# Performance work log

Measured on AMD Instinct MI355X. Metric: run time of the kernel, lower is better.

## Reference

```python
import jax, jax.numpy as jnp
import numpy as np

NU = 50000   # num user nodes
NI = 50000   # num item nodes
E = 1600000  # edges per relation
DIN = 256    # in_features
H = 8        # n_heads
F = 64       # out_features per head (hidden = H*F = 512)
NEG_SLOPE = 0.2


def setup_inputs() -> dict:
    key = jax.random.key(0)
    ks = jax.random.split(key, 14)
    wscale = 0.05
    return {
        "x_user": jax.random.normal(ks[0], (NU, DIN), jnp.float32),
        "x_item": jax.random.normal(ks[1], (NI, DIN), jnp.float32),
        "Wv": jax.random.normal(ks[2], (3, DIN, H * F), jnp.float32) * wscale,
        "bv": jax.random.normal(ks[3], (3, H * F), jnp.float32) * wscale,
        "Wq": jax.random.normal(ks[4], (3, H * F, H), jnp.float32) * wscale,
        "bq": jax.random.normal(ks[5], (3, H), jnp.float32) * wscale,
        "Wk": jax.random.normal(ks[6], (3, H * F, H), jnp.float32) * wscale,
        "bk": jax.random.normal(ks[7], (3, H), jnp.float32) * wscale,
        "src1": jax.random.randint(ks[8], (E,), 0, NU, jnp.int32),   # user -> item
        "dst1": jax.random.randint(ks[9], (E,), 0, NI, jnp.int32),
        "src2": jax.random.randint(ks[10], (E,), 0, NI, jnp.int32),  # item -> user
        "dst2": jax.random.randint(ks[11], (E,), 0, NU, jnp.int32),
        "src3": jax.random.randint(ks[12], (E,), 0, NU, jnp.int32),  # user -> user
        "dst3": jax.random.randint(ks[13], (E,), 0, NU, jnp.int32),
    }


def _gat_relation(x_src, x_dst, Wv, bv, Wq, bq, Wk, bk, src, dst, n_dst):
    # linear_v on src and dst node features: [N, H*F]
    h_src = x_src @ Wv + bv
    h_dst = x_dst @ Wv + bv
    q = h_dst @ Wq + bq  # [Nd, H] per-head query logit
    k = h_src @ Wk + bk  # [Ns, H] per-head key logit
    # fused_gsddmm: gather to edges, leaky_relu, segment softmax over dst
    e = jax.nn.leaky_relu(q[dst] + k[src], NEG_SLOPE)  # [E, H]
    m = jax.ops.segment_max(e, dst, num_segments=n_dst)  # [Nd, H]
    m = jnp.where(jnp.isfinite(m), m, jnp.zeros_like(m))
    ex = jnp.exp(e - m[dst])
    denom = jax.ops.segment_sum(ex, dst, num_segments=n_dst)  # [Nd, H]
    attn = ex / jnp.maximum(denom[dst], 1e-9)  # [E, H]
    # gspmm: attention-weighted scatter-sum of src features into dst
    hs = h_src.reshape(-1, H, F)  # [Ns, H, F]
    agg = jax.ops.segment_sum(attn[:, :, None] * hs[src], dst, num_segments=n_dst)  # [Nd, H, F]
    return agg.mean(axis=1)  # torch.mean(h, dim=1) -> [Nd, F]


def reference(x_user, x_item, Wv, bv, Wq, bq, Wk, bk, src1, dst1, src2, dst2, src3, dst3):
    # relation 0: user -> item
    out_item = _gat_relation(x_user, x_item, Wv[0], bv[0], Wq[0], bq[0], Wk[0], bk[0], src1, dst1, NI)
    # relations 1 (item -> user) and 2 (user -> user) both target user: mean over relations
    r1 = _gat_relation(x_item, x_user, Wv[1], bv[1], Wq[1], bq[1], Wk[1], bk[1], src2, dst2, NU)
    r2 = _gat_relation(x_user, x_user, Wv[2], bv[2], Wq[2], bq[2], Wk[2], bk[2], src3, dst3, NU)
    out_user = (r1 + r2) / 2.0
    return out_user, out_item
```

## Files before the change

### kernel.cpp

```cpp
#include <hip/hip_runtime.h>

typedef unsigned short u16;
typedef __attribute__((ext_vector_type(4))) float f32x4;
typedef __attribute__((ext_vector_type(8))) short s16x8;

#define NND 50000
#define EDG 1600000
#define NBK 391
#define TOTB (3 * NBK)
#define TS 4096

__device__ __forceinline__ u16 f2b(float f) {
  union { float f; unsigned u; } c; c.f = f;
  unsigned r = c.u + 0x7fff + ((c.u >> 16) & 1);
  return (u16)(r >> 16);
}
__device__ __forceinline__ float b2f(u16 b) {
  union { float f; unsigned u; } c; c.u = ((unsigned)b) << 16; return c.f;
}

__global__ void k_zero(int* p, int n) {
  int i = blockIdx.x * 256 + threadIdx.x;
  if (i < n) p[i] = 0;
}

__global__ void k_prepw(const float* __restrict__ Wv, u16* __restrict__ Wt) {
  int tid = blockIdx.x * 256 + threadIdx.x;
  if (tid < 3 * 512 * 256) {
    int r = tid / (512 * 256); int rem = tid - r * 512 * 256;
    int n = rem >> 8; int kk = rem & 255;
    Wt[tid] = f2b(Wv[((size_t)r * 256 + kk) * 512 + n]);
  }
}

__global__ void k_fusew(const float* __restrict__ Wv, const float* __restrict__ bv,
                        const float* __restrict__ Wq, const float* __restrict__ bq,
                        const float* __restrict__ Wk, const float* __restrict__ bk,
                        float* __restrict__ FW, float* __restrict__ FB) {
  int tid = blockIdx.x * 256 + threadIdx.x;
  if (tid < 3 * 16 * 256) {
    int r = tid >> 12, o = (tid >> 8) & 15, kk = tid & 255;
    const float* wv = Wv + ((size_t)r * 256 + kk) * 512;
    const float* wqk = (o < 8) ? (Wq + r * 512 * 8 + o) : (Wk + r * 512 * 8 + (o - 8));
    float s = 0.f;
    for (int j = 0; j < 512; j++) s += wv[j] * wqk[j * 8];
    FW[tid] = s;
  }
  if (tid < 48) {
    int r = tid / 16, o = tid % 16;
    const float* wqk = (o < 8) ? (Wq + r * 512 * 8 + o) : (Wk + r * 512 * 8 + (o - 8));
    const float* bvp = bv + r * 512;
    float s = (o < 8) ? bq[r * 8 + o] : bk[r * 8 + (o - 8)];
    for (int j = 0; j < 512; j++) s += bvp[j] * wqk[j * 8];
    FB[tid] = s;
  }
}


__global__ void kb_count(const int* __restrict__ d1, const int* __restrict__ d2,
                         const int* __restrict__ d3, int* __restrict__ BC) {
  __shared__ int h[NBK];
  int tid = threadIdx.x;
  int r = blockIdx.y;
  const int* d = (r == 0) ? d1 : (r == 1) ? d2 : d3;
  for (int b = tid; b < NBK; b += 256) h[b] = 0;
  __syncthreads();
  for (int e = blockIdx.x * 256 + tid; e < EDG; e += 256 * gridDim.x)
    atomicAdd(&h[d[e] >> 7], 1);
  __syncthreads();
  for (int b = tid; b < NBK; b += 256)
    if (h[b]) atomicAdd(&BC[r * NBK + b], h[b]);
}

__global__ void kb_scan(const int* __restrict__ BC, int* __restrict__ BB,
                        int* __restrict__ BCUR, int* __restrict__ rp) {
  __shared__ int a[2][2048];
  int t = threadIdx.x;
  a[0][t]        = (t < TOTB) ? BC[t] : 0;
  a[0][t + 1024] = (t + 1024 < TOTB) ? BC[t + 1024] : 0;
  __syncthreads();
  int s = 0;
  for (int off = 1; off < 2048; off <<= 1) {
    int v0 = a[s][t];        if (t >= off) v0 += a[s][t - off];
    int v1 = a[s][t + 1024]; if (t + 1024 >= off) v1 += a[s][t + 1024 - off];
    __syncthreads();
    a[s ^ 1][t] = v0; a[s ^ 1][t + 1024] = v1;
    __syncthreads();
    s ^= 1;
  }
  if (t < TOTB)        { int e = a[s][t] - BC[t];               BB[t] = e;        BCUR[t] = e; }
  if (t + 1024 < TOTB) { int e = a[s][t + 1024] - BC[t + 1024]; BB[t + 1024] = e; BCUR[t + 1024] = e; }
  if (t == 0) rp[3 * NND] = 3 * EDG;
}

__global__ void __launch_bounds__(256) kb_scatter(
    const int* __restrict__ s1, const int* __restrict__ d1,
    const int* __restrict__ s2, const int* __restrict__ d2,
    const int* __restrict__ s3, const int* __restrict__ d3,
    int* __restrict__ BCUR, unsigned* __restrict__ pairs) {
  __shared__ int h[NBK];
  __shared__ int bbase[NBK];
  int tid = threadIdx.x;
  int r = blockIdx.y;
  const int* dp = (r == 0) ? d1 : (r == 1) ? d2 : d3;
  const int* sp = (r == 0) ? s1 : (r == 1) ? s2 : s3;
  int e0 = blockIdx.x * TS;
  int n = EDG - e0; if (n > TS) n = TS;
  for (int b = tid; b < NBK; b += 256) h[b] = 0;
  __syncthreads();
  int eb[16]; unsigned ev[16];
#pragma unroll
  for (int k = 0; k < 16; k++) {
    int i = k * 256 + tid;
    if (i < n) {
      int d = dp[e0 + i], ss = sp[e0 + i];
      eb[k] = d >> 7;
      ev[k] = ((unsigned)(d & 127) << 16) | (unsigned)ss;
      atomicAdd(&h[eb[k]], 1);
    } else eb[k] = -1;
  }
  __syncthreads();
  for (int b = tid; b < NBK; b += 256) {
    int c = h[b];
    bbase[b] = c ? atomicAdd(&BCUR[r * NBK + b], c) : 0;
  }
  __syncthreads();
  for (int b = tid; b < NBK; b += 256) h[b] = 0;
  __syncthreads();
#pragma unroll
  for (int k = 0; k < 16; k++) {
    if (eb[k] >= 0) {
      int off = atomicAdd(&h[eb[k]], 1);
      pairs[bbase[eb[k]] + off] = ev[k];
    }
  }
}

__global__ void __launch_bounds__(256) kb_build(
    const unsigned* __restrict__ pairs, const int* __restrict__ BB,
    const int* __restrict__ BC, int* __restrict__ rp, int* __restrict__ csrc) {
  __shared__ int cntl[128];
  __shared__ int sc[128];
  __shared__ int curl[128];
  int t = threadIdx.x;
  int r = blockIdx.y, bx = blockIdx.x;
  int bin = r * NBK + bx;
  int base = BB[bin], cnt = BC[bin];
  int node0 = bx << 7;
  int nloc = NND - node0; if (nloc > 128) nloc = 128;
  if (t < 128) cntl[t] = 0;
  __syncthreads();
  for (int i = t; i < cnt; i += 256)
    atomicAdd(&cntl[pairs[base + i] >> 16], 1);
  __syncthreads();
  if (t < 128) sc[t] = cntl[t];
  __syncthreads();
  for (int off = 1; off < 128; off <<= 1) {
    int v = 0;
    if (t < 128) { v = sc[t]; if (t >= off) v += sc[t - off]; }
    __syncthreads();
    if (t < 128) sc[t] = v;
    __syncthreads();
  }
  if (t < 128) {
    int excl = sc[t] - cntl[t];
    if (t < nloc) rp[r * NND + node0 + t] = base + excl;
    curl[t] = base + excl;
  }
  __syncthreads();
  for (int i = t; i < cnt; i += 256) {
    unsigned v = pairs[base + i];
    int p = atomicAdd(&curl[v >> 16], 1);
    csrc[p] = (int)(v & 0xFFFFu);
  }
}

__global__ void __launch_bounds__(256) k_gemm(const float* __restrict__ A, const u16* __restrict__ Bt,
                                              const float* __restrict__ bias, u16* __restrict__ C, int M) {
  __shared__ u16 sA[128 * 40];
  __shared__ u16 sB[128 * 40];
  int tid = threadIdx.x;
  int lane = tid & 63, wid = tid >> 6;
  int wm = wid >> 1, wn = wid & 1;
  int l15 = lane & 15, l4 = lane >> 4;
  int m0 = blockIdx.x * 128, n0 = blockIdx.y * 128;
  f32x4 acc[4][4] = {};
  for (int ko = 0; ko < 256; ko += 32) {
#pragma unroll
    for (int p = 0; p < 2; p++) {
      int idx = p * 256 + tid;
      int row = idx >> 2, seg = idx & 3;
      int gm = m0 + row; if (gm >= M) gm = M - 1;
      float4 a0 = *(const float4*)(A + (size_t)gm * 256 + ko + seg * 8);
      float4 a1 = *(const float4*)(A + (size_t)gm * 256 + ko + seg * 8 + 4);
      s16x8 av;
      av[0] = (short)f2b(a0.x); av[1] = (short)f2b(a0.y);
      av[2] = (short)f2b(a0.z); av[3] = (short)f2b(a0.w);
      av[4] = (short)f2b(a1.x); av[5] = (short)f2b(a1.y);
      av[6] = (short)f2b(a1.z); av[7] = (short)f2b(a1.w);
      *(s16x8*)&sA[row * 40 + seg * 8] = av;
      *(s16x8*)&sB[row * 40 + seg * 8] = *(const s16x8*)(Bt + (n0 + row) * 256 + ko + seg * 8);
    }
    __syncthreads();
    s16x8 af[4], bf[4];
#pragma unroll
    for (int i = 0; i < 4; i++) af[i] = *(const s16x8*)&sA[(wm * 64 + i * 16 + l15) * 40 + l4 * 8];
#pragma unroll
    for (int j = 0; j < 4; j++) bf[j] = *(const s16x8*)&sB[(wn * 64 + j * 16 + l15) * 40 + l4 * 8];
#pragma unroll
    for (int i = 0; i < 4; i++)
#pragma unroll
      for (int j = 0; j < 4; j++)
        acc[i][j] = __builtin_amdgcn_mfma_f32_16x16x32_bf16(af[i], bf[j], acc[i][j], 0, 0, 0);
    __syncthreads();
  }
#pragma unroll
  for (int j = 0; j < 4; j++) {
    int n = n0 + wn * 64 + j * 16 + l15;
    float bb = bias[n];
#pragma unroll
    for (int i = 0; i < 4; i++) {
      int mb = m0 + wm * 64 + i * 16 + l4 * 4;
#pragma unroll
      for (int r = 0; r < 4; r++) {
        int m = mb + r;
        if (m < M) C[(size_t)m * 512 + n] = f2b(acc[i][j][r] + bb);
      }
    }
  }
}

__global__ void k_qk(const float* __restrict__ x, const float* __restrict__ FW,
                     const float* __restrict__ FB, float* __restrict__ qout,
                     float* __restrict__ kout, int N) {
  int lane = threadIdx.x & 63, wid = threadIdx.x >> 6;
  int stride = gridDim.x * 4;
  for (int row = blockIdx.x * 4 + wid; row < N; row += stride) {
    float4 xv = *(const float4*)(x + (size_t)row * 256 + lane * 4);
    float p[16];
#pragma unroll
    for (int o = 0; o < 16; o++) {
      float4 wv = *(const float4*)(FW + o * 256 + lane * 4);
      p[o] = xv.x * wv.x + xv.y * wv.y + xv.z * wv.z + xv.w * wv.w;
    }
#pragma unroll
    for (int off = 1; off < 64; off <<= 1)
#pragma unroll
      for (int o = 0; o < 16; o++) p[o] += __shfl_xor(p[o], off, 64);
    if (lane == 0) {
      if (qout) {
#pragma unroll
        for (int o = 0; o < 8; o++) qout[row * 8 + o] = p[o] + FB[o];
      }
      if (kout) {
#pragma unroll
        for (int o = 0; o < 8; o++) kout[row * 8 + o] = p[o + 8] + FB[o + 8];
      }
    }
  }
}

__global__ void __launch_bounds__(256) k_edge(const int* __restrict__ rp, const int* __restrict__ csrc,
                       const float* __restrict__ q, const float* __restrict__ k,
                       const u16* __restrict__ hs, float* __restrict__ out,
                       float scale, int accum) {
  __shared__ float exw[4][64 * 8];
  __shared__ int sarr[4][64];
  int lane = threadIdx.x & 63, w = threadIdx.x >> 6;
  int dst = blockIdx.x * 4 + w;
  if (dst >= NND) return;
  int beg = rp[dst];
  int deg = rp[dst + 1] - beg;
  float qv[8];
  {
    float4 q0 = *(const float4*)(q + dst * 8);
    float4 q1 = *(const float4*)(q + dst * 8 + 4);
    qv[0] = q0.x; qv[1] = q0.y; qv[2] = q0.z; qv[3] = q0.w;
    qv[4] = q1.x; qv[5] = q1.y; qv[6] = q1.z; qv[7] = q1.w;
  }
  float dsum[8] = {0, 0, 0, 0, 0, 0, 0, 0};
  for (int base = 0; base < deg; base += 64) {
    int i = base + lane;
    if (i < deg) {
      int s = csrc[beg + i];
      float4 k0 = *(const float4*)(k + s * 8);
      float4 k1 = *(const float4*)(k + s * 8 + 4);
      float kv[8] = {k0.x, k0.y, k0.z, k0.w, k1.x, k1.y, k1.z, k1.w};
#pragma unroll
      for (int h = 0; h < 8; h++) {
        float e = qv[h] + kv[h];
        e = e > 0.f ? e : 0.2f * e;
        dsum[h] += exp2f(e * 1.44269504f);
      }
    }
  }
#pragma unroll
  for (int off = 1; off < 64; off <<= 1)
#pragma unroll
    for (int h = 0; h < 8; h++) dsum[h] += __shfl_xor(dsum[h], off, 64);
  float rden[8];
#pragma unroll
  for (int h = 0; h < 8; h++) rden[h] = dsum[h] > 0.f ? 1.f / dsum[h] : 0.f;

  float acc8[8] = {0, 0, 0, 0, 0, 0, 0, 0};
  for (int base = 0; base < deg; base += 64) {
    int i = base + lane;
    int nn = min(64, deg - base);
    if (i < deg) {
      int s = csrc[beg + i];
      sarr[w][lane] = s;
      float4 k0 = *(const float4*)(k + s * 8);
      float4 k1 = *(const float4*)(k + s * 8 + 4);
      float kv[8] = {k0.x, k0.y, k0.z, k0.w, k1.x, k1.y, k1.z, k1.w};
#pragma unroll
      for (int h = 0; h < 8; h++) {
        float e = qv[h] + kv[h];
        e = e > 0.f ? e : 0.2f * e;
        exw[w][lane * 8 + h] = exp2f(e * 1.44269504f) * rden[h];
      }
    }
    __asm__ __volatile__("s_waitcnt lgkmcnt(0)" ::: "memory");
    for (int j = 0; j < nn; j++) {
      int s = sarr[w][j];
      const u16* hp = hs + (size_t)s * 512 + lane;
      float4 e0 = *(const float4*)&exw[w][j * 8];
      float4 e1 = *(const float4*)&exw[w][j * 8 + 4];
      acc8[0] += e0.x * b2f(hp[0 * 64]);
      acc8[1] += e0.y * b2f(hp[1 * 64]);
      acc8[2] += e0.z * b2f(hp[2 * 64]);
      acc8[3] += e0.w * b2f(hp[3 * 64]);
      acc8[4] += e1.x * b2f(hp[4 * 64]);
      acc8[5] += e1.y * b2f(hp[5 * 64]);
      acc8[6] += e1.z * b2f(hp[6 * 64]);
      acc8[7] += e1.w * b2f(hp[7 * 64]);
    }
  }
  float acc = ((acc8[0] + acc8[1]) + (acc8[2] + acc8[3])) + ((acc8[4] + acc8[5]) + (acc8[6] + acc8[7]));
  acc *= scale;
  if (accum) out[dst * 64 + lane] += acc;
  else out[dst * 64 + lane] = acc;
}

extern "C" void kernel_launch(void* const* d_in, const int* in_sizes, int n_in,
                              void* d_out, int out_size, void* d_ws, size_t ws_size,
                              hipStream_t stream) {
  const float* xu = (const float*)d_in[0];
  const float* xi = (const float*)d_in[1];
  const float* Wv = (const float*)d_in[2];
  const float* bv = (const float*)d_in[3];
  const float* Wq = (const float*)d_in[4];
  const float* bq = (const float*)d_in[5];
  const float* Wk = (const float*)d_in[6];
  const float* bk = (const float*)d_in[7];
  const int* src1 = (const int*)d_in[8];
  const int* dst1 = (const int*)d_in[9];
  const int* src2 = (const int*)d_in[10];
  const int* dst2 = (const int*)d_in[11];
  const int* src3 = (const int*)d_in[12];
  const int* dst3 = (const int*)d_in[13];
  float* out_user = (float*)d_out;
  float* out_item = out_user + (size_t)NND * 64;

  char* w = (char*)d_ws;
  auto alloc = [&](size_t sz) -> char* {
    char* p = w; w += (sz + 255) & ~(size_t)255; return p;
  };
  u16* H    = (u16*)alloc((size_t)NND * 512 * 2);
  u16* WT   = (u16*)alloc((size_t)3 * 512 * 256 * 2);
  float* FW = (float*)alloc((size_t)3 * 16 * 256 * 4);
  float* FB = (float*)alloc((size_t)3 * 16 * 4);
  float* Q0 = (float*)alloc((size_t)NND * 8 * 4);
  float* K0 = (float*)alloc((size_t)NND * 8 * 4);
  float* Q1 = (float*)alloc((size_t)NND * 8 * 4);
  float* K1 = (float*)alloc((size_t)NND * 8 * 4);
  float* Q2 = (float*)alloc((size_t)NND * 8 * 4);
  float* K2 = (float*)alloc((size_t)NND * 8 * 4);
  int* ROWPTR = (int*)alloc(((size_t)3 * NND + 1) * 4);
  int* BC   = (int*)alloc(TOTB * 4);
  int* BB   = (int*)alloc(TOTB * 4);
  int* BCUR = (int*)alloc(TOTB * 4);
  int* CSRC = (int*)alloc((size_t)3 * EDG * 4);
  unsigned* PAIRS = (unsigned*)H;
  (void)ws_size; (void)n_in; (void)in_sizes; (void)out_size;

  k_zero<<<(TOTB + 255) / 256, 256, 0, stream>>>(BC, TOTB);
  kb_count<<<dim3(256, 3), 256, 0, stream>>>(dst1, dst2, dst3, BC);
  kb_scan<<<1, 1024, 0, stream>>>(BC, BB, BCUR, ROWPTR);
  kb_scatter<<<dim3((EDG + TS - 1) / TS, 3), 256, 0, stream>>>(src1, dst1, src2, dst2, src3, dst3, BCUR, PAIRS);
  kb_build<<<dim3(NBK, 3), 256, 0, stream>>>(PAIRS, BB, BC, ROWPTR, CSRC);

  k_prepw<<<(3 * 512 * 256 + 255) / 256, 256, 0, stream>>>(Wv, WT);
  k_fusew<<<48, 256, 0, stream>>>(Wv, bv, Wq, bq, Wk, bk, FW, FB);

  k_qk<<<1024, 256, 0, stream>>>(xi, FW,        FB,      Q0, nullptr, NND);
  k_qk<<<1024, 256, 0, stream>>>(xu, FW,        FB,      nullptr, K0, NND);
  k_qk<<<1024, 256, 0, stream>>>(xu, FW + 4096, FB + 16, Q1, nullptr, NND);
  k_qk<<<1024, 256, 0, stream>>>(xi, FW + 4096, FB + 16, nullptr, K1, NND);
  k_qk<<<1024, 256, 0, stream>>>(xu, FW + 8192, FB + 32, Q2, K2, NND);

  dim3 gg((NND + 127) / 128, 4);
  k_gemm<<<gg, 256, 0, stream>>>(xu, WT,                 bv,        H, NND);
  k_edge<<<NND / 4, 256, 0, stream>>>(ROWPTR,           CSRC, Q0, K0, H, out_item, 0.125f,  0);
  k_gemm<<<gg, 256, 0, stream>>>(xi, WT + 512 * 256,     bv + 512,  H, NND);
  k_edge<<<NND / 4, 256, 0, stream>>>(ROWPTR + NND,     CSRC, Q1, K1, H, out_user, 0.0625f, 0);
  k_gemm<<<gg, 256, 0, stream>>>(xu, WT + 2 * 512 * 256, bv + 1024, H, NND);
  k_edge<<<NND / 4, 256, 0, stream>>>(ROWPTR + 2 * NND, CSRC, Q2, K2, H, out_user, 0.0625f, 1);
}
```

Measured before the change: 1.279 ms.

## Sort CSR bins in LDS, interleave GEMM output heads, fuse q/k projections

kb_build now loads each destination bin into shared memory and bitonic-sorts it, so CSR sources come out in deterministic sorted order; the old atomic path is kept as a fallback for oversized bins. The GEMM writes its output with head and feature interleaved, so each lane in k_edge can fetch its 8 per-head bf16 values with one 16-byte load instead of eight strided 2-byte loads. The five q/k projection launches are merged into two kernels, one per input matrix, so x_user and x_item are each read once. The bitonic sort adds many barrier-separated passes in kb_build, and the 32-output k_qk_u kernel raises register pressure.

```diff
diff --git a/kernel.cpp b/kernel.cpp
--- a/kernel.cpp
+++ b/kernel.cpp
@@ -9,6 +9,7 @@
 #define NBK 391
 #define TOTB (3 * NBK)
 #define TS 4096
+#define SCAP 8192
 
 __device__ __forceinline__ u16 f2b(float f) {
   union { float f; unsigned u; } c; c.f = f;
@@ -139,40 +140,68 @@
 __global__ void __launch_bounds__(256) kb_build(
     const unsigned* __restrict__ pairs, const int* __restrict__ BB,
     const int* __restrict__ BC, int* __restrict__ rp, int* __restrict__ csrc) {
-  __shared__ int cntl[128];
-  __shared__ int sc[128];
-  __shared__ int curl[128];
+  __shared__ unsigned A[SCAP];
   int t = threadIdx.x;
   int r = blockIdx.y, bx = blockIdx.x;
   int bin = r * NBK + bx;
   int base = BB[bin], cnt = BC[bin];
   int node0 = bx << 7;
   int nloc = NND - node0; if (nloc > 128) nloc = 128;
-  if (t < 128) cntl[t] = 0;
-  __syncthreads();
-  for (int i = t; i < cnt; i += 256)
-    atomicAdd(&cntl[pairs[base + i] >> 16], 1);
-  __syncthreads();
-  if (t < 128) sc[t] = cntl[t];
-  __syncthreads();
-  for (int off = 1; off < 128; off <<= 1) {
-    int v = 0;
-    if (t < 128) { v = sc[t]; if (t >= off) v += sc[t - off]; }
-    __syncthreads();
-    if (t < 128) sc[t] = v;
-    __syncthreads();
-  }
-  if (t < 128) {
-    int excl = sc[t] - cntl[t];
-    if (t < nloc) rp[r * NND + node0 + t] = base + excl;
-    curl[t] = base + excl;
-  }
-  __syncthreads();
+
+  if (cnt > SCAP) {
+    int* cntl = (int*)A; int* sc = (int*)A + 128; int* curl = (int*)A + 256;
+    if (t < 128) cntl[t] = 0;
+    __syncthreads();
+    for (int i = t; i < cnt; i += 256) atomicAdd(&cntl[pairs[base + i] >> 16], 1);
+    __syncthreads();
+    if (t < 128) sc[t] = cntl[t];
+    __syncthreads();
+    for (int off = 1; off < 128; off <<= 1) {
+      int v = 0;
+      if (t < 128) { v = sc[t]; if (t >= off) v += sc[t - off]; }
+      __syncthreads();
+      if (t < 128) sc[t] = v;
+      __syncthreads();
+    }
+    if (t < 128) {
+      int excl = sc[t] - cntl[t];
+      if (t < nloc) rp[r * NND + node0 + t] = base + excl;
+      curl[t] = base + excl;
+    }
+    __syncthreads();
+    for (int i = t; i < cnt; i += 256) {
+      unsigned v = pairs[base + i];
+      int p = atomicAdd(&curl[v >> 16], 1);
+      csrc[p] = (int)(v & 0xFFFFu);
+    }
+    return;
+  }
+
+  int n = 1024; while (n < cnt) n <<= 1;
+  for (int i = t; i < n; i += 256) A[i] = (i < cnt) ? pairs[base + i] : 0xFFFFFFFFu;
+  __syncthreads();
+  for (int ksz = 2; ksz <= n; ksz <<= 1) {
+    for (int j = ksz >> 1; j > 0; j >>= 1) {
+      for (int i = t; i < n; i += 256) {
+        int p = i ^ j;
+        if (p > i) {
+          unsigned a = A[i], b = A[p];
+          bool up = ((i & ksz) == 0);
+          if ((a > b) == up) { A[i] = b; A[p] = a; }
+        }
+      }
+      __syncthreads();
+    }
+  }
   for (int i = t; i < cnt; i += 256) {
-    unsigned v = pairs[base + i];
-    int p = atomicAdd(&curl[v >> 16], 1);
-    csrc[p] = (int)(v & 0xFFFFu);
-  }
+    unsigned key = A[i];
+    int d = (int)(key >> 16);
+    int dprev = (i == 0) ? -1 : (int)(A[i - 1] >> 16);
+    for (int x = dprev + 1; x <= d; x++) rp[r * NND + node0 + x] = base + i;
+    csrc[base + i] = (int)(key & 0xFFFFu);
+  }
+  int dlast = (cnt > 0) ? (int)(A[cnt - 1] >> 16) : -1;
+  for (int x = dlast + 1 + t; x < nloc; x += 256) rp[r * NND + node0 + x] = base + cnt;
 }
 
 __global__ void __launch_bounds__(256) k_gemm(const float* __restrict__ A, const u16* __restrict__ Bt,
@@ -218,44 +247,74 @@
   for (int j = 0; j < 4; j++) {
     int n = n0 + wn * 64 + j * 16 + l15;
     float bb = bias[n];
+    int tpos = ((n & 63) << 3) + (n >> 6);
 #pragma unroll
     for (int i = 0; i < 4; i++) {
       int mb = m0 + wm * 64 + i * 16 + l4 * 4;
 #pragma unroll
       for (int r = 0; r < 4; r++) {
         int m = mb + r;
-        if (m < M) C[(size_t)m * 512 + n] = f2b(acc[i][j][r] + bb);
+        if (m < M) C[(size_t)m * 512 + tpos] = f2b(acc[i][j][r] + bb);
       }
     }
   }
 }
 
-__global__ void k_qk(const float* __restrict__ x, const float* __restrict__ FW,
-                     const float* __restrict__ FB, float* __restrict__ qout,
-                     float* __restrict__ kout, int N) {
+__global__ void k_qk_u(const float* __restrict__ x, const float* __restrict__ FW,
+                       const float* __restrict__ FB, float* __restrict__ K0,
+                       float* __restrict__ Q1, float* __restrict__ Q2,
+                       float* __restrict__ K2, int N) {
+  int lane = threadIdx.x & 63, wid = threadIdx.x >> 6;
+  int stride = gridDim.x * 4;
+  for (int row = blockIdx.x * 4 + wid; row < N; row += stride) {
+    float4 xv = *(const float4*)(x + (size_t)row * 256 + lane * 4);
+    float p[32];
+#pragma unroll
+    for (int c = 0; c < 32; c++) {
+      int o = (c < 8) ? (8 + c) : (c < 16) ? (4096 / 256 * 16 + (c - 8)) : (2 * 16 + (c - 16));
+      const float4 wv = *(const float4*)(FW + (size_t)((c < 8) ? (8 + c) : (c < 16) ? (16 + (c - 8)) : (32 + (c - 16))) * 256 + lane * 4);
+      p[c] = xv.x * wv.x + xv.y * wv.y + xv.z * wv.z + xv.w * wv.w;
+      (void)o;
+    }
+#pragma unroll
+    for (int off = 1; off < 64; off <<= 1)
+#pragma unroll
+      for (int c = 0; c < 32; c++) p[c] += __shfl_xor(p[c], off, 64);
+    if (lane == 0) {
+#pragma unroll
+      for (int c = 0; c < 8; c++) K0[row * 8 + c] = p[c] + FB[8 + c];
+#pragma unroll
+      for (int c = 0; c < 8; c++) Q1[row * 8 + c] = p[8 + c] + FB[16 + c];
+#pragma unroll
+      for (int c = 0; c < 8; c++) Q2[row * 8 + c] = p[16 + c] + FB[32 + c];
+#pragma unroll
+      for (int c = 0; c < 8; c++) K2[row * 8 + c] = p[24 + c] + FB[40 + c];
+    }
+  }
+}
+
+__global__ void k_qk_i(const float* __restrict__ x, const float* __restrict__ FW,
+                       const float* __restrict__ FB, float* __restrict__ Q0,
+                       float* __restrict__ K1, int N) {
   int lane = threadIdx.x & 63, wid = threadIdx.x >> 6;
   int stride = gridDim.x * 4;
   for (int row = blockIdx.x * 4 + wid; row < N; row += stride) {
     float4 xv = *(const float4*)(x + (size_t)row * 256 + lane * 4);
     float p[16];
 #pragma unroll
-    for (int o = 0; o < 16; o++) {
-      float4 wv = *(const float4*)(FW + o * 256 + lane * 4);
-      p[o] = xv.x * wv.x + xv.y * wv.y + xv.z * wv.z + xv.w * wv.w;
+    for (int c = 0; c < 16; c++) {
+      const float4 wv = *(const float4*)(FW + (size_t)((c < 8) ? c : (16 + c)) * 256 + lane * 4);
+      p[c] = xv.x * wv.x + xv.y * wv.y + xv.z * wv.z + xv.w * wv.w;
     }
 #pragma unroll
     for (int off = 1; off < 64; off <<= 1)
 #pragma unroll
-      for (int o = 0; o < 16; o++) p[o] += __shfl_xor(p[o], off, 64);
+      for (int c = 0; c < 16; c++) p[c] += __shfl_xor(p[c], off, 64);
     if (lane == 0) {
-      if (qout) {
-#pragma unroll
-        for (int o = 0; o < 8; o++) qout[row * 8 + o] = p[o] + FB[o];
-      }
-      if (kout) {
-#pragma unroll
-        for (int o = 0; o < 8; o++) kout[row * 8 + o] = p[o + 8] + FB[o + 8];
-      }
+#pragma unroll
+      for (int c = 0; c < 8; c++) Q0[row * 8 + c] = p[c] + FB[c];
+#pragma unroll
+      for (int c = 0; c < 8; c++) K1[row * 8 + c] = p[8 + c] + FB[24 + c];
     }
   }
 }
@@ -322,17 +381,17 @@
     __asm__ __volatile__("s_waitcnt lgkmcnt(0)" ::: "memory");
     for (int j = 0; j < nn; j++) {
       int s = sarr[w][j];
-      const u16* hp = hs + (size_t)s * 512 + lane;
+      s16x8 hv = *(const s16x8*)(hs + (size_t)s * 512 + lane * 8);
       float4 e0 = *(const float4*)&exw[w][j * 8];
       float4 e1 = *(const float4*)&exw[w][j * 8 + 4];
-      acc8[0] += e0.x * b2f(hp[0 * 64]);
-      acc8[1] += e0.y * b2f(hp[1 * 64]);
-      acc8[2] += e0.z * b2f(hp[2 * 64]);
-      acc8[3] += e0.w * b2f(hp[3 * 64]);
-      acc8[4] += e1.x * b2f(hp[4 * 64]);
-      acc8[5] += e1.y * b2f(hp[5 * 64]);
-      acc8[6] += e1.z * b2f(hp[6 * 64]);
-      acc8[7] += e1.w * b2f(hp[7 * 64]);
+      acc8[0] += e0.x * b2f((u16)hv[0]);
+      acc8[1] += e0.y * b2f((u16)hv[1]);
+      acc8[2] += e0.z * b2f((u16)hv[2]);
+      acc8[3] += e0.w * b2f((u16)hv[3]);
+      acc8[4] += e1.x * b2f((u16)hv[4]);
+      acc8[5] += e1.y * b2f((u16)hv[5]);
+      acc8[6] += e1.z * b2f((u16)hv[6]);
+      acc8[7] += e1.w * b2f((u16)hv[7]);
     }
   }
   float acc = ((acc8[0] + acc8[1]) + (acc8[2] + acc8[3])) + ((acc8[4] + acc8[5]) + (acc8[6] + acc8[7]));
@@ -392,11 +451,8 @@
   k_prepw<<<(3 * 512 * 256 + 255) / 256, 256, 0, stream>>>(Wv, WT);
   k_fusew<<<48, 256, 0, stream>>>(Wv, bv, Wq, bq, Wk, bk, FW, FB);
 
-  k_qk<<<1024, 256, 0, stream>>>(xi, FW,        FB,      Q0, nullptr, NND);
-  k_qk<<<1024, 256, 0, stream>>>(xu, FW,        FB,      nullptr, K0, NND);
-  k_qk<<<1024, 256, 0, stream>>>(xu, FW + 4096, FB + 16, Q1, nullptr, NND);
-  k_qk<<<1024, 256, 0, stream>>>(xi, FW + 4096, FB + 16, nullptr, K1, NND);
-  k_qk<<<1024, 256, 0, stream>>>(xu, FW + 8192, FB + 32, Q2, K2, NND);
+  k_qk_u<<<1024, 256, 0, stream>>>(xu, FW, FB, K0, Q1, Q2, K2, NND);
+  k_qk_i<<<1024, 256, 0, stream>>>(xi, FW, FB, Q0, K1, NND);
 
   dim3 gg((NND + 127) / 128, 4);
   k_gemm<<<gg, 256, 0, stream>>>(xu, WT,                 bv,        H, NND);
```

Measured after the change: 1.809 ms. 1.41x slower.
